# Kernel tuning notes

Hardware: AMD Instinct MI355X
Metric: run time of the kernel (lower is better)

The kernel has to match this reference:

```python
import jax, jax.numpy as jnp
import numpy as np

D = 1024        # model dim
H = 8           # num heads
HD = D // H     # head dim = 128
EPS = 1e-6
B, L = 2, 4096


def _rmsnorm(x, g):
    # RMSNorm over the full model dim (applied before head split, as in source)
    return x * jax.lax.rsqrt(jnp.mean(x * x, axis=-1, keepdims=True) + EPS) * g


def _rope_interleaved(x, cos, sin):
    # x: [B, L, H, HD]; cos/sin: [L, HD//2]
    x1 = x[..., 0::2]
    x2 = x[..., 1::2]
    c = cos[None, :, None, :]
    s = sin[None, :, None, :]
    # interleave (x1*c - x2*s, x1*s + x2*c) back into even/odd lanes
    out = jnp.stack([x1 * c - x2 * s, x1 * s + x2 * c], axis=-1)
    return out.reshape(x.shape)


def setup_inputs() -> dict:
    key = jax.random.key(0)
    ks = jax.random.split(key, 6)
    x = jax.random.normal(ks[0], (B, L, D), dtype=jnp.float32)
    freqs_cos = jax.random.uniform(ks[1], (L, HD // 2), dtype=jnp.float32)
    freqs_sin = jax.random.uniform(ks[2], (L, HD // 2), dtype=jnp.float32)
    s = 1.0 / np.sqrt(D).astype(np.float32)
    w_qkv = jax.random.normal(ks[3], (D, 3 * D), dtype=jnp.float32) * s
    b_qkv = jnp.zeros((3 * D,), dtype=jnp.float32)
    g_q = jnp.ones((D,), dtype=jnp.float32)
    g_k = jnp.ones((D,), dtype=jnp.float32)
    w_out = jax.random.normal(ks[4], (D, D), dtype=jnp.float32) * s
    b_out = jnp.zeros((D,), dtype=jnp.float32)
    return {"x": x, "freqs_cos": freqs_cos, "freqs_sin": freqs_sin,
            "w_qkv": w_qkv, "b_qkv": b_qkv, "g_q": g_q, "g_k": g_k,
            "w_out": w_out, "b_out": b_out}


def reference(x, freqs_cos, freqs_sin, w_qkv, b_qkv, g_q, g_k, w_out, b_out):
    Bx, Lx, _ = x.shape
    qkv = x @ w_qkv + b_qkv                      # [B, L, 3D]
    q, k, v = jnp.split(qkv, 3, axis=-1)          # each [B, L, D]
    q = _rmsnorm(q, g_q)
    k = _rmsnorm(k, g_k)
    q = q.reshape(Bx, Lx, H, HD)
    k = k.reshape(Bx, Lx, H, HD)
    v = v.reshape(Bx, Lx, H, HD)
    q = _rope_interleaved(q, freqs_cos, freqs_sin)
    k = _rope_interleaved(k, freqs_cos, freqs_sin)
    scale = 1.0 / np.sqrt(HD)
    scores = jnp.einsum('blhd,bmhd->bhlm', q, k) * scale
    attn = jax.nn.softmax(scores, axis=-1)
    o = jnp.einsum('bhlm,bmhd->blhd', attn, v).reshape(Bx, Lx, D)
    return o @ w_out + b_out
```

## Files before the change

### kernel.cpp

```cpp
#include <hip/hip_runtime.h>
#include <hip/hip_bf16.h>
#include <stdint.h>

typedef __attribute__((ext_vector_type(8))) short short8;
typedef __attribute__((ext_vector_type(4))) short short4v;
typedef __attribute__((ext_vector_type(4))) float f32x4;
typedef __attribute__((ext_vector_type(16))) float f32x16;

#define LSEQ 4096
#define DMODEL 1024
#define NHEAD 8
#define HDIM 128
#define MTOT 8192
#define NQKV 3072

__device__ __forceinline__ unsigned short f2bf(float f){
  unsigned u = __float_as_uint(f);
  u += 0x7fffu + ((u >> 16) & 1u);
  return (unsigned short)(u >> 16);
}
__device__ __forceinline__ float bf2f(unsigned short h){
  return __uint_as_float(((unsigned)h) << 16);
}

typedef const __attribute__((address_space(1))) void* gas_ptr;
typedef __attribute__((address_space(3))) void* las_ptr;
__device__ __forceinline__ void gload_lds16(const void* g, void* l){
  __builtin_amdgcn_global_load_lds((gas_ptr)(uintptr_t)g,
                                   (las_ptr)(unsigned)(uintptr_t)l, 16, 0, 0);
}

__global__ __launch_bounds__(256) void k_cvt(const float* __restrict__ in,
                                             unsigned short* __restrict__ out, int n8){
  int i = blockIdx.x*256 + threadIdx.x;
  if (i >= n8) return;
  const float4* p = (const float4*)in + (size_t)i*2;
  float4 a = p[0], b = p[1];
  short8 r;
  r[0]=(short)f2bf(a.x); r[1]=(short)f2bf(a.y); r[2]=(short)f2bf(a.z); r[3]=(short)f2bf(a.w);
  r[4]=(short)f2bf(b.x); r[5]=(short)f2bf(b.y); r[6]=(short)f2bf(b.z); r[7]=(short)f2bf(b.w);
  *(short8*)(out + (size_t)i*8) = r;
}

__global__ __launch_bounds__(256) void k_transpose_cvt(const float* __restrict__ in,
                                                       unsigned short* __restrict__ out,
                                                       int R, int C){
  __shared__ unsigned short tile[32][33];
  int c0 = blockIdx.x*32, r0 = blockIdx.y*32;
  int tx = threadIdx.x & 31, ty = threadIdx.x >> 5;
  #pragma unroll
  for (int i=0;i<32;i+=8)
    tile[ty+i][tx] = f2bf(in[(size_t)(r0+ty+i)*C + c0+tx]);
  __syncthreads();
  #pragma unroll
  for (int i=0;i<32;i+=8)
    out[(size_t)(c0+ty+i)*R + r0+tx] = tile[tx][ty+i];
}

__global__ __launch_bounds__(256) void k_vT(const unsigned short* __restrict__ qkv,
                                            unsigned short* __restrict__ vT){
  __shared__ unsigned short tile[32][33];
  int bh = blockIdx.z; int b = bh >> 3, h = bh & 7;
  int l0 = blockIdx.x*32, d0 = blockIdx.y*32;
  const unsigned short* src = qkv + (size_t)b*LSEQ*NQKV + 2*DMODEL + h*HDIM;
  int tx = threadIdx.x & 31, ty = threadIdx.x >> 5;
  #pragma unroll
  for (int i=0;i<32;i+=8)
    tile[ty+i][tx] = src[(size_t)(l0+ty+i)*NQKV + d0+tx];
  __syncthreads();
  unsigned short* dst = vT + ((size_t)bh*HDIM + d0)*LSEQ + l0;
  #pragma unroll
  for (int i=0;i<32;i+=8)
    dst[(size_t)(ty+i)*LSEQ + tx] = tile[tx][ty+i];
}

template<int OUT_BF16>
__global__ __launch_bounds__(256) void k_gemm_bt(const unsigned short* __restrict__ A,
                                                 const unsigned short* __restrict__ Bt,
                                                 const float* __restrict__ bias,
                                                 void* __restrict__ Cout,
                                                 int M, int N, int K){
  __shared__ unsigned short As[128*64];
  __shared__ unsigned short Bs[128*64];
  int tid = threadIdx.x, lane = tid & 63, wave = tid >> 6;
  int wm = wave >> 1, wn = wave & 1;
  int m0 = blockIdx.y*128, n0 = blockIdx.x*128;
  f32x4 zero = {0.f,0.f,0.f,0.f};
  f32x4 acc[4][4];
  #pragma unroll
  for (int mi=0;mi<4;++mi)
    #pragma unroll
    for (int ni=0;ni<4;++ni) acc[mi][ni] = zero;

  int srow = lane >> 3;
  int soffb = (lane & 7) * 16;
  int scol = (soffb ^ (srow << 4)) >> 1;
  int cg = lane >> 4, cl = lane & 15;

  int nkt = K >> 6;
  for (int kt = 0; kt < nkt; ++kt){
    if (kt) __syncthreads();
    int kbase = kt*64;
    #pragma unroll
    for (int j=0;j<4;++j){
      int ch = wave*4 + j;
      int row = ch*8 + srow;
      gload_lds16(A  + (size_t)(m0+row)*K + kbase + scol, (char*)As + ch*1024);
      gload_lds16(Bt + (size_t)(n0+row)*K + kbase + scol, (char*)Bs + ch*1024);
    }
    __syncthreads();

    short8 af[4][2], bf[4][2];
    #pragma unroll
    for (int mi=0;mi<4;++mi){
      int row = wm*64 + mi*16 + cl;
      int key = (row & 7) << 4;
      #pragma unroll
      for (int kk=0;kk<2;++kk)
        af[mi][kk] = *(const short8*)((const char*)As + row*128 + ((kk*64 + cg*16) ^ key));
    }
    #pragma unroll
    for (int ni=0;ni<4;++ni){
      int row = wn*64 + ni*16 + cl;
      int key = (row & 7) << 4;
      #pragma unroll
      for (int kk=0;kk<2;++kk)
        bf[ni][kk] = *(const short8*)((const char*)Bs + row*128 + ((kk*64 + cg*16) ^ key));
    }
    #pragma unroll
    for (int kk=0;kk<2;++kk)
      #pragma unroll
      for (int mi=0;mi<4;++mi)
        #pragma unroll
        for (int ni=0;ni<4;++ni)
          acc[mi][ni] = __builtin_amdgcn_mfma_f32_16x16x32_bf16(af[mi][kk], bf[ni][kk], acc[mi][ni], 0,0,0);
  }

  #pragma unroll
  for (int ni=0;ni<4;++ni){
    int col = n0 + wn*64 + ni*16 + cl;
    float bv = bias[col];
    #pragma unroll
    for (int mi=0;mi<4;++mi){
      int r = m0 + wm*64 + mi*16 + cg*4;
      #pragma unroll
      for (int i=0;i<4;++i){
        float v = acc[mi][ni][i] + bv;
        if (OUT_BF16) ((unsigned short*)Cout)[(size_t)(r+i)*N + col] = f2bf(v);
        else          ((float*)Cout)[(size_t)(r+i)*N + col] = v;
      }
    }
  }
}

__global__ __launch_bounds__(256) void k_norm_rope(unsigned short* __restrict__ qkv,
                                                   const float* __restrict__ fcos,
                                                   const float* __restrict__ fsin,
                                                   const float* __restrict__ gq,
                                                   const float* __restrict__ gk){
  int bl = blockIdx.x;
  int l = bl & (LSEQ-1);
  int t = threadIdx.x;
  unsigned short* row = qkv + (size_t)bl * NQKV;
  int d0 = t*4;
  short4v qv = *(short4v*)(row + d0);
  short4v kv = *(short4v*)(row + DMODEL + d0);
  float q[4], k[4];
  #pragma unroll
  for (int j=0;j<4;++j){ q[j] = bf2f((unsigned short)qv[j]); k[j] = bf2f((unsigned short)kv[j]); }
  float sq = q[0]*q[0]+q[1]*q[1]+q[2]*q[2]+q[3]*q[3];
  float sk = k[0]*k[0]+k[1]*k[1]+k[2]*k[2]+k[3]*k[3];
  #pragma unroll
  for (int o=32;o;o>>=1){ sq += __shfl_xor(sq,o); sk += __shfl_xor(sk,o); }
  __shared__ float red[8];
  int lane = t & 63, wv = t >> 6;
  if (!lane){ red[wv] = sq; red[4+wv] = sk; }
  __syncthreads();
  sq = red[0]+red[1]+red[2]+red[3];
  sk = red[4]+red[5]+red[6]+red[7];
  float rq = rsqrtf(sq*(1.f/1024.f) + 1e-6f);
  float rk = rsqrtf(sk*(1.f/1024.f) + 1e-6f);
  int hd = d0 & (HDIM-1);
  int fi = (l << 6) + (hd >> 1);
  float c0 = fcos[fi], s0 = fsin[fi], c1 = fcos[fi+1], s1 = fsin[fi+1];
  {
    float x1 = q[0]*rq*gq[d0],   x2 = q[1]*rq*gq[d0+1];
    float x3 = q[2]*rq*gq[d0+2], x4 = q[3]*rq*gq[d0+3];
    short4v qo;
    qo[0]=(short)f2bf(x1*c0 - x2*s0); qo[1]=(short)f2bf(x1*s0 + x2*c0);
    qo[2]=(short)f2bf(x3*c1 - x4*s1); qo[3]=(short)f2bf(x3*s1 + x4*c1);
    *(short4v*)(row + d0) = qo;
  }
  {
    float x1 = k[0]*rk*gk[d0],   x2 = k[1]*rk*gk[d0+1];
    float x3 = k[2]*rk*gk[d0+2], x4 = k[3]*rk*gk[d0+3];
    short4v ko;
    ko[0]=(short)f2bf(x1*c0 - x2*s0); ko[1]=(short)f2bf(x1*s0 + x2*c0);
    ko[2]=(short)f2bf(x3*c1 - x4*s1); ko[3]=(short)f2bf(x3*s1 + x4*c1);
    *(short4v*)(row + DMODEL + d0) = ko;
  }
}

__global__ __launch_bounds__(256, 2) void k_attn(const unsigned short* __restrict__ qkv,
                                                 const unsigned short* __restrict__ vT,
                                                 unsigned short* __restrict__ o){
  __shared__ unsigned short Ks[2][64*128];
  __shared__ unsigned short VTs[2][128*64];
  int bh = blockIdx.y; int b = bh >> 3, h = bh & 7;
  int q0 = blockIdx.x * 128;
  int tid = threadIdx.x, lane = tid & 63, wave = tid >> 6;
  int ql = lane & 31, hf = lane >> 5;
  const unsigned short* base = qkv + (size_t)b*LSEQ*NQKV + h*HDIM;
  const unsigned short* kgl = base + DMODEL;
  const unsigned short* vtg = vT + (size_t)bh*HDIM*LSEQ;

  short8 qf[8];
  {
    const unsigned short* qr = base + (size_t)(q0 + wave*32 + ql)*NQKV + hf*8;
    #pragma unroll
    for (int st=0;st<8;++st) qf[st] = *(const short8*)(qr + st*16);
  }

  const float K2 = 0.12753568849800323f;
  float mrow = -3.0e38f, lrow = 0.f;
  f32x16 z16 = {0.f};
  f32x16 acc[4];
  acc[0]=z16; acc[1]=z16; acc[2]=z16; acc[3]=z16;

  int key = (ql & 7) << 4;

  int k_row4 = lane >> 4;
  (void)k_row4;
  int v_dl   = lane >> 3;
  int v_srcb = ((lane & 7)*16) ^ (v_dl << 4);
  int cgk = (lane >> 4) & 3;

  #pragma unroll
  for (int j=0;j<4;++j){
    int ch = wave*4 + j;
    int row = ch*4 + cgk;
    int srcb = ((lane & 15)*16) ^ ((row & 7) << 4);
    gload_lds16(kgl + (size_t)row*NQKV + (srcb >> 1), (char*)Ks[0] + ch*1024);
  }
  #pragma unroll
  for (int j=0;j<4;++j){
    int ch = wave*4 + j;
    int d = ch*8 + v_dl;
    gload_lds16(vtg + (size_t)d*LSEQ + (v_srcb >> 1), (char*)VTs[0] + ch*1024);
  }

  const int NT = LSEQ/64;
  for (int t = 0; t < NT; ++t){
    int cur = t & 1;
    __syncthreads();

    if (t+1 < NT){
      int kvn = (t+1)*64;
      #pragma unroll
      for (int j=0;j<4;++j){
        int ch = wave*4 + j;
        int row = ch*4 + cgk;
        int srcb = ((lane & 15)*16) ^ ((row & 7) << 4);
        gload_lds16(kgl + (size_t)(kvn+row)*NQKV + (srcb >> 1), (char*)Ks[cur^1] + ch*1024);
      }
      #pragma unroll
      for (int j=0;j<4;++j){
        int ch = wave*4 + j;
        int d = ch*8 + v_dl;
        gload_lds16(vtg + (size_t)d*LSEQ + kvn + (v_srcb >> 1), (char*)VTs[cur^1] + ch*1024);
      }
    }

    const char* kb = (const char*)Ks[cur];
    const char* vb = (const char*)VTs[cur];

    f32x16 s0 = z16, s1 = z16;
    __builtin_amdgcn_s_setprio(1);
    #pragma unroll
    for (int st=0;st<8;++st){
      int col = (hf*16 + st*32) ^ key;
      short8 kf0 = *(const short8*)(kb + ql*256 + col);
      short8 kf1 = *(const short8*)(kb + ql*256 + 8192 + col);
      s0 = __builtin_amdgcn_mfma_f32_32x32x16_bf16(kf0, qf[st], s0, 0,0,0);
      s1 = __builtin_amdgcn_mfma_f32_32x32x16_bf16(kf1, qf[st], s1, 0,0,0);
    }
    __builtin_amdgcn_s_setprio(0);

    float mx = s0[0];
    #pragma unroll
    for (int i=1;i<16;++i) mx = fmaxf(mx, s0[i]);
    #pragma unroll
    for (int i=0;i<16;++i) mx = fmaxf(mx, s1[i]);
    mx = fmaxf(mx, __shfl_xor(mx, 32));
    float mx2 = mx * K2;
    bool rescale = !__all(mx2 <= mrow + 11.5416f);
    if (rescale){
      float mn = fmaxf(mrow, mx2);
      float fac = exp2f(mrow - mn);
      mrow = mn;
      lrow *= fac;
      float fr[16];
      #pragma unroll
      for (int r=0;r<16;++r) fr[r] = __shfl(fac, (r&3) + 8*(r>>2) + 4*hf);
      #pragma unroll
      for (int dt=0;dt<4;++dt)
        #pragma unroll
        for (int r=0;r<16;++r) acc[dt][r] *= fr[r];
    }
    float sum = 0.f;
    #pragma unroll
    for (int i=0;i<16;++i){
      float e = exp2f(fmaf(s0[i], K2, -mrow));
      s0[i] = e; sum += e;
    }
    #pragma unroll
    for (int i=0;i<16;++i){
      float e = exp2f(fmaf(s1[i], K2, -mrow));
      s1[i] = e; sum += e;
    }
    lrow += sum;

    __builtin_amdgcn_s_setprio(1);
    #pragma unroll
    for (int c=0;c<4;++c){
      unsigned c01, c23, c45, c67;
      if (c < 2){
        int rb = (c&1)*8;
        asm("v_cvt_pk_bf16_f32 %0, %1, %2" : "=v"(c01) : "v"(s0[rb+0]), "v"(s0[rb+1]));
        asm("v_cvt_pk_bf16_f32 %0, %1, %2" : "=v"(c23) : "v"(s0[rb+2]), "v"(s0[rb+3]));
        asm("v_cvt_pk_bf16_f32 %0, %1, %2" : "=v"(c45) : "v"(s0[rb+4]), "v"(s0[rb+5]));
        asm("v_cvt_pk_bf16_f32 %0, %1, %2" : "=v"(c67) : "v"(s0[rb+6]), "v"(s0[rb+7]));
      } else {
        int rb = (c&1)*8;
        asm("v_cvt_pk_bf16_f32 %0, %1, %2" : "=v"(c01) : "v"(s1[rb+0]), "v"(s1[rb+1]));
        asm("v_cvt_pk_bf16_f32 %0, %1, %2" : "=v"(c23) : "v"(s1[rb+2]), "v"(s1[rb+3]));
        asm("v_cvt_pk_bf16_f32 %0, %1, %2" : "=v"(c45) : "v"(s1[rb+4]), "v"(s1[rb+5]));
        asm("v_cvt_pk_bf16_f32 %0, %1, %2" : "=v"(c67) : "v"(s1[rb+6]), "v"(s1[rb+7]));
      }
      asm("v_permlane32_swap_b32 %0, %1" : "+v"(c01), "+v"(c45));
      asm("v_permlane32_swap_b32 %0, %1" : "+v"(c23), "+v"(c67));
      union { unsigned u[4]; short8 v; } pu;
      pu.u[0] = c01; pu.u[1] = c23; pu.u[2] = c45; pu.u[3] = c67;
      short8 pa = pu.v;
      #pragma unroll
      for (int dt=0;dt<4;++dt){
        int col = (c*32 + hf*16) ^ key;
        short8 vf = *(const short8*)(vb + (dt*32 + ql)*128 + col);
        acc[dt] = __builtin_amdgcn_mfma_f32_32x32x16_bf16(pa, vf, acc[dt], 0,0,0);
      }
    }
    __builtin_amdgcn_s_setprio(0);
  }

  lrow += __shfl_xor(lrow, 32);
  float rl = 1.f / lrow;
  float rr[16];
  #pragma unroll
  for (int r=0;r<16;++r) rr[r] = __shfl(rl, (r&3) + 8*(r>>2) + 4*hf);
  size_t qbase = (size_t)(b*LSEQ + q0 + wave*32);
  #pragma unroll
  for (int dt=0;dt<4;++dt){
    int col = h*HDIM + dt*32 + ql;
    #pragma unroll
    for (int r=0;r<16;++r){
      int qrow = (r&3) + 8*(r>>2) + 4*hf;
      o[(qbase + qrow)*DMODEL + col] = f2bf(acc[dt][r]*rr[r]);
    }
  }
}

extern "C" void kernel_launch(void* const* d_in, const int* in_sizes, int n_in,
                              void* d_out, int out_size, void* d_ws, size_t ws_size,
                              hipStream_t stream) {
  const float* x    = (const float*)d_in[0];
  const float* fcos = (const float*)d_in[1];
  const float* fsin = (const float*)d_in[2];
  const float* wqkv = (const float*)d_in[3];
  const float* bqkv = (const float*)d_in[4];
  const float* gq   = (const float*)d_in[5];
  const float* gk   = (const float*)d_in[6];
  const float* wout = (const float*)d_in[7];
  const float* bout = (const float*)d_in[8];
  float* out = (float*)d_out;

  char* ws = (char*)d_ws;
  unsigned short* xb    = (unsigned short*)(ws);
  unsigned short* qkv   = (unsigned short*)(ws + (16ull<<20));
  unsigned short* ob    = (unsigned short*)(ws + (64ull<<20));
  unsigned short* wqkvT = (unsigned short*)(ws + (80ull<<20));
  unsigned short* woutT = (unsigned short*)(ws + (86ull<<20));
  unsigned short* vT    = xb;

  k_cvt<<<4096, 256, 0, stream>>>(x, xb, (MTOT*DMODEL)/8);
  k_transpose_cvt<<<dim3(96,32), 256, 0, stream>>>(wqkv, wqkvT, DMODEL, NQKV);
  k_transpose_cvt<<<dim3(32,32), 256, 0, stream>>>(wout, woutT, DMODEL, DMODEL);
  k_gemm_bt<1><<<dim3(NQKV/128, MTOT/128), 256, 0, stream>>>(xb, wqkvT, bqkv, qkv, MTOT, NQKV, DMODEL);
  k_norm_rope<<<MTOT, 256, 0, stream>>>(qkv, fcos, fsin, gq, gk);
  k_vT<<<dim3(LSEQ/32, HDIM/32, 16), 256, 0, stream>>>(qkv, vT);
  k_attn<<<dim3(LSEQ/128, 16), 256, 0, stream>>>(qkv, vT, ob);
  k_gemm_bt<0><<<dim3(DMODEL/128, MTOT/128), 256, 0, stream>>>(ob, woutT, bout, out, MTOT, DMODEL, DMODEL);
}
```

Before: 301.2 us.

## Compute softmax row sums via MFMA with ones vector and use v_max3 reductions

Replaces the per-lane scalar accumulation of exp values with an extra MFMA per 32-key chunk that multiplies the bf16 probabilities by a ones operand. The row sums then land directly in the accumulator layout, so the final shuffles are no longer needed. The row-max reduction now uses v_max3_f32 in a tree to cut VALU instructions. The denominator is now summed from bf16-rounded probabilities, which matches the numerator's precision, but it adds MFMA work and 16 accumulator registers.

```diff
diff --git a/kernel.cpp b/kernel.cpp
--- a/kernel.cpp
+++ b/kernel.cpp
@@ -21,6 +21,11 @@
 }
 __device__ __forceinline__ float bf2f(unsigned short h){
   return __uint_as_float(((unsigned)h) << 16);
+}
+__device__ __forceinline__ float max3f(float a, float b, float c){
+  float d;
+  asm("v_max3_f32 %0, %1, %2, %3" : "=v"(d) : "v"(a), "v"(b), "v"(c));
+  return d;
 }
 
 typedef const __attribute__((address_space(1))) void* gas_ptr;
@@ -220,17 +225,19 @@
     #pragma unroll
     for (int st=0;st<8;++st) qf[st] = *(const short8*)(qr + st*16);
   }
+  short8 ones;
+  #pragma unroll
+  for (int j=0;j<8;++j) ones[j] = (short)0x3F80;
 
   const float K2 = 0.12753568849800323f;
-  float mrow = -3.0e38f, lrow = 0.f;
+  float mrow = -3.0e38f;
   f32x16 z16 = {0.f};
   f32x16 acc[4];
   acc[0]=z16; acc[1]=z16; acc[2]=z16; acc[3]=z16;
+  f32x16 accl = z16;
 
   int key = (ql & 7) << 4;
 
-  int k_row4 = lane >> 4;
-  (void)k_row4;
   int v_dl   = lane >> 3;
   int v_srcb = ((lane & 7)*16) ^ (v_dl << 4);
   int cgk = (lane >> 4) & 3;
@@ -286,19 +293,25 @@
     }
     __builtin_amdgcn_s_setprio(0);
 
-    float mx = s0[0];
-    #pragma unroll
-    for (int i=1;i<16;++i) mx = fmaxf(mx, s0[i]);
-    #pragma unroll
-    for (int i=0;i<16;++i) mx = fmaxf(mx, s1[i]);
+    float t10[10];
+    #pragma unroll
+    for (int j=0;j<5;++j)  t10[j]   = max3f(s0[3*j], s0[3*j+1], s0[3*j+2]);
+    t10[5] = max3f(s0[15], s1[0], s1[1]);
+    #pragma unroll
+    for (int j=0;j<4;++j)  t10[6+j] = max3f(s1[2+3*j], s1[3+3*j], s1[4+3*j]);
+    float u0 = max3f(t10[0], t10[1], t10[2]);
+    float u1 = max3f(t10[3], t10[4], t10[5]);
+    float u2 = max3f(t10[6], t10[7], t10[8]);
+    float u3 = max3f(t10[9], s1[14], s1[15]);
+    float mx = fmaxf(fmaxf(u0,u1), fmaxf(u2,u3));
     mx = fmaxf(mx, __shfl_xor(mx, 32));
+
     float mx2 = mx * K2;
     bool rescale = !__all(mx2 <= mrow + 11.5416f);
     if (rescale){
       float mn = fmaxf(mrow, mx2);
       float fac = exp2f(mrow - mn);
       mrow = mn;
-      lrow *= fac;
       float fr[16];
       #pragma unroll
       for (int r=0;r<16;++r) fr[r] = __shfl(fac, (r&3) + 8*(r>>2) + 4*hf);
@@ -306,19 +319,13 @@
       for (int dt=0;dt<4;++dt)
         #pragma unroll
         for (int r=0;r<16;++r) acc[dt][r] *= fr[r];
-    }
-    float sum = 0.f;
-    #pragma unroll
-    for (int i=0;i<16;++i){
-      float e = exp2f(fmaf(s0[i], K2, -mrow));
-      s0[i] = e; sum += e;
-    }
-    #pragma unroll
-    for (int i=0;i<16;++i){
-      float e = exp2f(fmaf(s1[i], K2, -mrow));
-      s1[i] = e; sum += e;
-    }
-    lrow += sum;
+      #pragma unroll
+      for (int r=0;r<16;++r) accl[r] *= fr[r];
+    }
+    #pragma unroll
+    for (int i=0;i<16;++i) s0[i] = exp2f(fmaf(s0[i], K2, -mrow));
+    #pragma unroll
+    for (int i=0;i<16;++i) s1[i] = exp2f(fmaf(s1[i], K2, -mrow));
 
     __builtin_amdgcn_s_setprio(1);
     #pragma unroll
@@ -342,6 +349,7 @@
       union { unsigned u[4]; short8 v; } pu;
       pu.u[0] = c01; pu.u[1] = c23; pu.u[2] = c45; pu.u[3] = c67;
       short8 pa = pu.v;
+      accl = __builtin_amdgcn_mfma_f32_32x32x16_bf16(pa, ones, accl, 0,0,0);
       #pragma unroll
       for (int dt=0;dt<4;++dt){
         int col = (c*32 + hf*16) ^ key;
@@ -352,11 +360,9 @@
     __builtin_amdgcn_s_setprio(0);
   }
 
-  lrow += __shfl_xor(lrow, 32);
-  float rl = 1.f / lrow;
   float rr[16];
   #pragma unroll
-  for (int r=0;r<16;++r) rr[r] = __shfl(rl, (r&3) + 8*(r>>2) + 4*hf);
+  for (int r=0;r<16;++r) rr[r] = 1.f / accl[r];
   size_t qbase = (size_t)(b*LSEQ + q0 + wave*32);
   #pragma unroll
   for (int dt=0;dt<4;++dt){
```

Result: faster. 294.6 us (-2.2%).

## Split attention KV tile across wave pairs with LDS merge of partial softmax

Applied to the files above, without the earlier changes.

Doubles the attention block to 512 threads. Each pair of waves shares a 32-row query block and splits every 64-key tile into two 32-key halves, so each wave keeps one score accumulator instead of two. At the end the two partial results are merged through LDS using their running max and sum, which adds an extra synchronisation and an exp-weighted combine. The max reduction also switches to v_max3_f32, and the goal is more waves in flight with lower register pressure per wave.

```diff
diff --git a/kernel.cpp b/kernel.cpp
--- a/kernel.cpp
+++ b/kernel.cpp
@@ -21,6 +21,11 @@
 }
 __device__ __forceinline__ float bf2f(unsigned short h){
   return __uint_as_float(((unsigned)h) << 16);
+}
+__device__ __forceinline__ float max3f(float a, float b, float c){
+  float d;
+  asm("v_max3_f32 %0, %1, %2, %3" : "=v"(d) : "v"(a), "v"(b), "v"(c));
+  return d;
 }
 
 typedef const __attribute__((address_space(1))) void* gas_ptr;
@@ -201,14 +206,19 @@
   }
 }
 
-__global__ __launch_bounds__(256, 2) void k_attn(const unsigned short* __restrict__ qkv,
+__global__ __launch_bounds__(512, 4) void k_attn(const unsigned short* __restrict__ qkv,
                                                  const unsigned short* __restrict__ vT,
                                                  unsigned short* __restrict__ o){
-  __shared__ unsigned short Ks[2][64*128];
-  __shared__ unsigned short VTs[2][128*64];
+  __shared__ char smem[68608];
+  unsigned short* Ks0 = (unsigned short*)smem;
+  unsigned short* VTs0 = (unsigned short*)(smem + 32768);
+  float* mO = (float*)smem;
+  float* mML = (float*)(smem + 65536);
+
   int bh = blockIdx.y; int b = bh >> 3, h = bh & 7;
   int q0 = blockIdx.x * 128;
   int tid = threadIdx.x, lane = tid & 63, wave = tid >> 6;
+  int qb = wave >> 1, kh = wave & 1;
   int ql = lane & 31, hf = lane >> 5;
   const unsigned short* base = qkv + (size_t)b*LSEQ*NQKV + h*HDIM;
   const unsigned short* kgl = base + DMODEL;
@@ -216,7 +226,7 @@
 
   short8 qf[8];
   {
-    const unsigned short* qr = base + (size_t)(q0 + wave*32 + ql)*NQKV + hf*8;
+    const unsigned short* qr = base + (size_t)(q0 + qb*32 + ql)*NQKV + hf*8;
     #pragma unroll
     for (int st=0;st<8;++st) qf[st] = *(const short8*)(qr + st*16);
   }
@@ -229,24 +239,22 @@
 
   int key = (ql & 7) << 4;
 
-  int k_row4 = lane >> 4;
-  (void)k_row4;
   int v_dl   = lane >> 3;
   int v_srcb = ((lane & 7)*16) ^ (v_dl << 4);
   int cgk = (lane >> 4) & 3;
 
   #pragma unroll
-  for (int j=0;j<4;++j){
-    int ch = wave*4 + j;
+  for (int j=0;j<2;++j){
+    int ch = wave*2 + j;
     int row = ch*4 + cgk;
     int srcb = ((lane & 15)*16) ^ ((row & 7) << 4);
-    gload_lds16(kgl + (size_t)row*NQKV + (srcb >> 1), (char*)Ks[0] + ch*1024);
-  }
-  #pragma unroll
-  for (int j=0;j<4;++j){
-    int ch = wave*4 + j;
+    gload_lds16(kgl + (size_t)row*NQKV + (srcb >> 1), (char*)Ks0 + ch*1024);
+  }
+  #pragma unroll
+  for (int j=0;j<2;++j){
+    int ch = wave*2 + j;
     int d = ch*8 + v_dl;
-    gload_lds16(vtg + (size_t)d*LSEQ + (v_srcb >> 1), (char*)VTs[0] + ch*1024);
+    gload_lds16(vtg + (size_t)d*LSEQ + (v_srcb >> 1), (char*)VTs0 + ch*1024);
   }
 
   const int NT = LSEQ/64;
@@ -257,41 +265,43 @@
     if (t+1 < NT){
       int kvn = (t+1)*64;
       #pragma unroll
-      for (int j=0;j<4;++j){
-        int ch = wave*4 + j;
+      for (int j=0;j<2;++j){
+        int ch = wave*2 + j;
         int row = ch*4 + cgk;
         int srcb = ((lane & 15)*16) ^ ((row & 7) << 4);
-        gload_lds16(kgl + (size_t)(kvn+row)*NQKV + (srcb >> 1), (char*)Ks[cur^1] + ch*1024);
+        gload_lds16(kgl + (size_t)(kvn+row)*NQKV + (srcb >> 1),
+                    (char*)Ks0 + (cur^1)*16384 + ch*1024);
       }
       #pragma unroll
-      for (int j=0;j<4;++j){
-        int ch = wave*4 + j;
+      for (int j=0;j<2;++j){
+        int ch = wave*2 + j;
         int d = ch*8 + v_dl;
-        gload_lds16(vtg + (size_t)d*LSEQ + kvn + (v_srcb >> 1), (char*)VTs[cur^1] + ch*1024);
+        gload_lds16(vtg + (size_t)d*LSEQ + kvn + (v_srcb >> 1),
+                    (char*)VTs0 + (cur^1)*16384 + ch*1024);
       }
     }
 
-    const char* kb = (const char*)Ks[cur];
-    const char* vb = (const char*)VTs[cur];
-
-    f32x16 s0 = z16, s1 = z16;
+    const char* kb = (const char*)Ks0 + cur*16384;
+    const char* vb = (const char*)VTs0 + cur*16384;
+
+    f32x16 s0 = z16;
     __builtin_amdgcn_s_setprio(1);
     #pragma unroll
     for (int st=0;st<8;++st){
       int col = (hf*16 + st*32) ^ key;
-      short8 kf0 = *(const short8*)(kb + ql*256 + col);
-      short8 kf1 = *(const short8*)(kb + ql*256 + 8192 + col);
-      s0 = __builtin_amdgcn_mfma_f32_32x32x16_bf16(kf0, qf[st], s0, 0,0,0);
-      s1 = __builtin_amdgcn_mfma_f32_32x32x16_bf16(kf1, qf[st], s1, 0,0,0);
+      short8 kf = *(const short8*)(kb + (kh*32 + ql)*256 + col);
+      s0 = __builtin_amdgcn_mfma_f32_32x32x16_bf16(kf, qf[st], s0, 0,0,0);
     }
     __builtin_amdgcn_s_setprio(0);
 
-    float mx = s0[0];
-    #pragma unroll
-    for (int i=1;i<16;++i) mx = fmaxf(mx, s0[i]);
-    #pragma unroll
-    for (int i=0;i<16;++i) mx = fmaxf(mx, s1[i]);
+    float t0 = max3f(s0[0], s0[1], s0[2]);
+    float t1 = max3f(s0[3], s0[4], s0[5]);
+    float t2 = max3f(s0[6], s0[7], s0[8]);
+    float t3 = max3f(s0[9], s0[10], s0[11]);
+    float t4 = max3f(s0[12], s0[13], s0[14]);
+    float mx = max3f(max3f(t0, t1, t2), max3f(t3, t4, s0[15]), -3.0e38f);
     mx = fmaxf(mx, __shfl_xor(mx, 32));
+
     float mx2 = mx * K2;
     bool rescale = !__all(mx2 <= mrow + 11.5416f);
     if (rescale){
@@ -299,13 +309,11 @@
       float fac = exp2f(mrow - mn);
       mrow = mn;
       lrow *= fac;
-      float fr[16];
-      #pragma unroll
-      for (int r=0;r<16;++r) fr[r] = __shfl(fac, (r&3) + 8*(r>>2) + 4*hf);
       #pragma unroll
       for (int dt=0;dt<4;++dt)
         #pragma unroll
-        for (int r=0;r<16;++r) acc[dt][r] *= fr[r];
+        for (int r=0;r<16;++r)
+          acc[dt][r] *= __shfl(fac, (r&3) + 8*(r>>2) + 4*hf);
     }
     float sum = 0.f;
     #pragma unroll
@@ -313,30 +321,17 @@
       float e = exp2f(fmaf(s0[i], K2, -mrow));
       s0[i] = e; sum += e;
     }
-    #pragma unroll
-    for (int i=0;i<16;++i){
-      float e = exp2f(fmaf(s1[i], K2, -mrow));
-      s1[i] = e; sum += e;
-    }
     lrow += sum;
 
     __builtin_amdgcn_s_setprio(1);
     #pragma unroll
-    for (int c=0;c<4;++c){
+    for (int c=0;c<2;++c){
       unsigned c01, c23, c45, c67;
-      if (c < 2){
-        int rb = (c&1)*8;
-        asm("v_cvt_pk_bf16_f32 %0, %1, %2" : "=v"(c01) : "v"(s0[rb+0]), "v"(s0[rb+1]));
-        asm("v_cvt_pk_bf16_f32 %0, %1, %2" : "=v"(c23) : "v"(s0[rb+2]), "v"(s0[rb+3]));
-        asm("v_cvt_pk_bf16_f32 %0, %1, %2" : "=v"(c45) : "v"(s0[rb+4]), "v"(s0[rb+5]));
-        asm("v_cvt_pk_bf16_f32 %0, %1, %2" : "=v"(c67) : "v"(s0[rb+6]), "v"(s0[rb+7]));
-      } else {
-        int rb = (c&1)*8;
-        asm("v_cvt_pk_bf16_f32 %0, %1, %2" : "=v"(c01) : "v"(s1[rb+0]), "v"(s1[rb+1]));
-        asm("v_cvt_pk_bf16_f32 %0, %1, %2" : "=v"(c23) : "v"(s1[rb+2]), "v"(s1[rb+3]));
-        asm("v_cvt_pk_bf16_f32 %0, %1, %2" : "=v"(c45) : "v"(s1[rb+4]), "v"(s1[rb+5]));
-        asm("v_cvt_pk_bf16_f32 %0, %1, %2" : "=v"(c67) : "v"(s1[rb+6]), "v"(s1[rb+7]));
-      }
+      int rb = c*8;
+      asm("v_cvt_pk_bf16_f32 %0, %1, %2" : "=v"(c01) : "v"(s0[rb+0]), "v"(s0[rb+1]));
+      asm("v_cvt_pk_bf16_f32 %0, %1, %2" : "=v"(c23) : "v"(s0[rb+2]), "v"(s0[rb+3]));
+      asm("v_cvt_pk_bf16_f32 %0, %1, %2" : "=v"(c45) : "v"(s0[rb+4]), "v"(s0[rb+5]));
+      asm("v_cvt_pk_bf16_f32 %0, %1, %2" : "=v"(c67) : "v"(s0[rb+6]), "v"(s0[rb+7]));
       asm("v_permlane32_swap_b32 %0, %1" : "+v"(c01), "+v"(c45));
       asm("v_permlane32_swap_b32 %0, %1" : "+v"(c23), "+v"(c67));
       union { unsigned u[4]; short8 v; } pu;
@@ -344,7 +339,7 @@
       short8 pa = pu.v;
       #pragma unroll
       for (int dt=0;dt<4;++dt){
-        int col = (c*32 + hf*16) ^ key;
+        int col = (kh*64 + c*32 + hf*16) ^ key;
         short8 vf = *(const short8*)(vb + (dt*32 + ql)*128 + col);
         acc[dt] = __builtin_amdgcn_mfma_f32_32x32x16_bf16(pa, vf, acc[dt], 0,0,0);
       }
@@ -353,18 +348,42 @@
   }
 
   lrow += __shfl_xor(lrow, 32);
-  float rl = 1.f / lrow;
-  float rr[16];
-  #pragma unroll
-  for (int r=0;r<16;++r) rr[r] = __shfl(rl, (r&3) + 8*(r>>2) + 4*hf);
-  size_t qbase = (size_t)(b*LSEQ + q0 + wave*32);
-  #pragma unroll
-  for (int dt=0;dt<4;++dt){
+  __syncthreads();
+
+  #pragma unroll
+  for (int i=0;i<2;++i){
+    int dt = (kh^1)*2 + i;
+    #pragma unroll
+    for (int rq=0;rq<4;++rq){
+      f32x4 w = { acc[dt][rq*4+0], acc[dt][rq*4+1], acc[dt][rq*4+2], acc[dt][rq*4+3] };
+      *(f32x4*)((char*)mO + ((qb*4 + dt)*4 + rq)*1024 + lane*16) = w;
+    }
+  }
+  mML[((qb*2 + kh)*32 + ql)*2 + 0] = mrow;
+  mML[((qb*2 + kh)*32 + ql)*2 + 1] = lrow;
+  __syncthreads();
+
+  size_t qbase = (size_t)(b*LSEQ + q0 + qb*32);
+  #pragma unroll
+  for (int i=0;i<2;++i){
+    int dt = kh*2 + i;
+    f32x4 ob[4];
+    #pragma unroll
+    for (int rq=0;rq<4;++rq)
+      ob[rq] = *(const f32x4*)((const char*)mO + ((qb*4 + dt)*4 + rq)*1024 + lane*16);
     int col = h*HDIM + dt*32 + ql;
     #pragma unroll
     for (int r=0;r<16;++r){
       int qrow = (r&3) + 8*(r>>2) + 4*hf;
-      o[(qbase + qrow)*DMODEL + col] = f2bf(acc[dt][r]*rr[r]);
+      float ma = __shfl(mrow, qrow);
+      float la = __shfl(lrow, qrow);
+      float mb = mML[((qb*2 + (kh^1))*32 + qrow)*2 + 0];
+      float lb = mML[((qb*2 + (kh^1))*32 + qrow)*2 + 1];
+      float m = fmaxf(ma, mb);
+      float ea = exp2f(ma - m), eb = exp2f(mb - m);
+      float denom = la*ea + lb*eb;
+      float v = (acc[dt][r]*ea + ob[r>>2][r&3]*eb) / denom;
+      o[(qbase + qrow)*DMODEL + col] = f2bf(v);
     }
   }
 }
@@ -397,6 +416,6 @@
   k_gemm_bt<1><<<dim3(NQKV/128, MTOT/128), 256, 0, stream>>>(xb, wqkvT, bqkv, qkv, MTOT, NQKV, DMODEL);
   k_norm_rope<<<MTOT, 256, 0, stream>>>(qkv, fcos, fsin, gq, gk);
   k_vT<<<dim3(LSEQ/32, HDIM/32, 16), 256, 0, stream>>>(qkv, vT);
-  k_attn<<<dim3(LSEQ/128, 16), 256, 0, stream>>>(qkv, vT, ob);
+  k_attn<<<dim3(LSEQ/128, 16), 512, 0, stream>>>(qkv, vT, ob);
   k_gemm_bt<0><<<dim3(DMODEL/128, MTOT/128), 256, 0, stream>>>(ob, woutT, bout, out, MTOT, DMODEL, DMODEL);
 }
```

After: 1.076 ms. 3.57x slower.
